# Kernel optimization log

Measured on AMD Instinct MI355X. Metric: run time of the kernel, lower is better.

The kernel has to match this reference:

```python
import jax, jax.numpy as jnp
import numpy as np

S = 1          # MD_S
R = 8          # MD_R
STEPS = 4      # MD_STEPS (train == eval)
INV_T = 1.0    # INV_T
EPS = 1e-6     # get_epsilon() for fp32, no params


def _build_estimators(D):
    # Smooth RBF basis bank: sigmas (6,8) stride 1, (12,15) stride 2, (18,24) stride 3, + ones column.
    t = jnp.arange(D, dtype=jnp.float32)[:, None]
    n = jnp.arange(D, dtype=jnp.float32)[None, :]
    dd = (t - n) ** 2
    cols = []
    for sig, stride in [(6.0, 1), (8.0, 1), (12.0, 2), (15.0, 2), (18.0, 3), (24.0, 3)]:
        rbf = jnp.exp(-0.5 * dd / (2.0 * sig * sig))
        cols.append(rbf[:, ::stride])
    cols.append(jnp.ones((D, 1), dtype=jnp.float32))
    return jnp.concatenate(cols, axis=1)  # [D, K], K = 589 for D = 160


def _l2_normalize(v, axis):
    # matches F.normalize(eps=1e-12)
    return v / jnp.maximum(jnp.linalg.norm(v, axis=axis, keepdims=True), 1e-12)


def _local_step(x, E, bases, coef):
    # NMF multiplicative update with smoothness estimators E (SNMF). x:[b,D,N], E:[b,D,K], bases:[b,K,R], coef:[b,N,R]
    Eb = jnp.einsum('bdk,bkr->bdr', E, bases)                      # [b,D,R]
    num_c = jnp.einsum('bdn,bdr->bnr', x, Eb)                      # x^T (E bases)
    den_c = jnp.einsum('bnr,brs->bns', coef, jnp.einsum('bdr,bds->brs', Eb, Eb))
    coef = coef * num_c / (den_c + EPS)
    num_b = jnp.einsum('bdk,bdr->bkr', E, jnp.einsum('bdn,bnr->bdr', x, coef))  # E^T (x coef)
    ctc = jnp.einsum('bnr,bns->brs', coef, coef)                   # [b,R,R]
    tmp = jnp.einsum('bdk,bkr->bdr', E, jnp.einsum('bkr,brs->bks', bases, ctc))
    den_b = jnp.einsum('bdk,bdr->bkr', E, tmp)                     # E^T E bases (coef^T coef)
    bases = bases * num_b / (den_b + EPS)
    return bases, coef


def _forward(x, bases_init):
    B, C, T, H, W = x.shape
    D = T // S
    N = C * H * W
    xr = x.reshape(B * S, D, N)                                    # same row-major view as torch .view
    E1 = _build_estimators(D)                                      # [D,K]
    E = jnp.broadcast_to(E1, (B * S,) + E1.shape)                  # [b,D,K]
    bases = _l2_normalize(bases_init, axis=1)                      # _build_bases: rand + normalize(dim=1)
    # local_inference (@torch.no_grad())
    Eb = jnp.einsum('bdk,bkr->bdr', E, bases)
    coef = jax.nn.softmax(INV_T * jnp.einsum('bdn,bdr->bnr', xr, Eb), axis=-1)
    for _ in range(STEPS):
        bases, coef = _local_step(xr, E, bases, coef)
    bases = jax.lax.stop_gradient(bases)
    coef = jax.lax.stop_gradient(coef)
    # compute_coef (differentiable single coef update)
    Eb = jnp.einsum('bdk,bkr->bdr', E, bases)
    num_c = jnp.einsum('bdn,bdr->bnr', xr, Eb)
    den_c = jnp.einsum('bnr,brs->bns', coef, jnp.einsum('bdr,bds->brs', Eb, Eb))
    coef = coef * num_c / (den_c + EPS)
    # reconstruction: (E bases) coef^T
    x_rec = jnp.einsum('bdr,bnr->bdn', Eb, coef)
    return x_rec.reshape(B, C, T, H, W)


def setup_inputs() -> dict:
    key = jax.random.key(0)
    k1, k2 = jax.random.split(key)
    B, C, T, H, W = 8, 32, 160, 32, 32
    D = T // S
    K = _build_estimators(D).shape[1]  # 589
    x = jax.random.uniform(k1, (B, C, T, H, W), dtype=jnp.float32)
    bases_init = jax.random.uniform(k2, (B * S, K, R), dtype=jnp.float32)
    return {"x": x, "bases_init": bases_init}


def reference(x, bases_init):
    return _forward(x, bases_init)
```

## Files before the change

### kernel.cpp

```cpp
#include <hip/hip_runtime.h>

#define DD   160
#define KKE  589
#define RR   8
#define NNX  32768
#define NB   8
#define EPSN 1e-6f

__global__ __launch_bounds__(256) void k_build(float* __restrict__ E, float* __restrict__ ET) {
    const int t = blockIdx.x;
    for (int j = threadIdx.x; j < KKE; j += 256) {
        float val;
        if (j == 588) {
            val = 1.f;
        } else {
            int n; float s2x4;
            if (j < 160)      { n = j;           s2x4 = 144.f;  }
            else if (j < 320) { n = j - 160;     s2x4 = 256.f;  }
            else if (j < 400) { n = 2*(j - 320); s2x4 = 576.f;  }
            else if (j < 480) { n = 2*(j - 400); s2x4 = 900.f;  }
            else if (j < 534) { n = 3*(j - 480); s2x4 = 1296.f; }
            else              { n = 3*(j - 534); s2x4 = 2304.f; }
            float d = (float)(t - n);
            val = expf(-(d * d) / s2x4);
        }
        E[t*KKE + j]  = val;
        ET[j*DD + t]  = val;
    }
}

template <bool NORM>
__global__ __launch_bounds__(256) void k_eb(const float* __restrict__ ET,
                                            const float* __restrict__ bsrc,
                                            float* __restrict__ bnorm_out,
                                            float* __restrict__ Eb_out,
                                            float* __restrict__ xc,
                                            float* __restrict__ ctc) {
    __shared__ float bcol[KKE];
    __shared__ float etch[64 * DD];
    __shared__ float red[4];
    const int tid = threadIdx.x;
    const int b = blockIdx.x >> 3;
    const int r = blockIdx.x & 7;

    const int k0 = tid, k1 = tid + 256, k2 = tid + 512;
    float v0 = bsrc[(b*KKE + k0)*RR + r];
    float v1 = bsrc[(b*KKE + k1)*RR + r];
    float v2 = (k2 < KKE) ? bsrc[(b*KKE + k2)*RR + r] : 0.f;

    if (NORM) {
        float ss = v0*v0 + v1*v1 + v2*v2;
        #pragma unroll
        for (int off = 32; off; off >>= 1) ss += __shfl_xor(ss, off);
        if ((tid & 63) == 0) red[tid >> 6] = ss;
        __syncthreads();
        float tot = red[0] + red[1] + red[2] + red[3];
        float scale = 1.f / fmaxf(sqrtf(tot), 1e-12f);
        v0 *= scale; v1 *= scale; v2 *= scale;
        bnorm_out[(b*KKE + k0)*RR + r] = v0;
        bnorm_out[(b*KKE + k1)*RR + r] = v1;
        if (k2 < KKE) bnorm_out[(b*KKE + k2)*RR + r] = v2;
    }
    bcol[k0] = v0; bcol[k1] = v1; if (k2 < KKE) bcol[k2] = v2;
    __syncthreads();

    float acc = 0.f;
    for (int c0 = 0; c0 < KKE; c0 += 64) {
        const int kcn = (KKE - c0 < 64) ? (KKE - c0) : 64;
        const int nf4 = kcn * (DD/4);
        for (int i4 = tid; i4 < nf4; i4 += 256)
            *(float4*)&etch[i4*4] = *(const float4*)&ET[c0*DD + i4*4];
        __syncthreads();
        if (tid < DD) {
            #pragma unroll 4
            for (int kk = 0; kk < kcn; ++kk)
                acc += etch[kk*DD + tid] * bcol[c0 + kk];
        }
        __syncthreads();
    }
    if (tid < DD) {
        Eb_out[b*DD*RR + tid*RR + r] = acc;
        xc[b*DD*RR + tid*RR + r] = 0.f;
    }
    if (tid < 8) ctc[b*64 + tid*8 + r] = 0.f;
}

template <bool FIRST>
__global__ __launch_bounds__(256) void k_step(const float* __restrict__ x,
                                              const float* __restrict__ Eb_g,
                                              float* __restrict__ coef,
                                              float* __restrict__ xc,
                                              float* __restrict__ ctc) {
    __shared__ float eb[DD*RR];
    __shared__ float ebteb[64];
    __shared__ float xt[64*161];
    __shared__ float pn[1536];

    const int tid = threadIdx.x;
    const int b = blockIdx.y;
    const int base_n = blockIdx.x * 256;

    for (int i = tid; i < DD*RR; i += 256) eb[i] = Eb_g[b*DD*RR + i];
    __syncthreads();
    if (tid < 64) {
        const int r = tid >> 3, s = tid & 7;
        float a = 0.f;
        #pragma unroll 4
        for (int d = 0; d < DD; ++d) a += eb[d*RR + r] * eb[d*RR + s];
        ebteb[tid] = a;
    }
    __syncthreads();

    float xcp[8] = {0,0,0,0,0,0,0,0};
    float ctcp = 0.f;

    const int q = tid >> 6;
    const int c = tid & 63;

    for (int st = 0; st < 4; ++st) {
        const int n0 = base_n + st*64;
        #pragma unroll
        for (int it = 0; it < 10; ++it) {
            const int idx = tid + it*256;
            const int row = idx >> 4;
            const int c4  = (idx & 15) << 2;
            const float4 v = *(const float4*)&x[(b*DD + row)*NNX + n0 + c4];
            xt[(c4+0)*161 + row] = v.x;
            xt[(c4+1)*161 + row] = v.y;
            xt[(c4+2)*161 + row] = v.z;
            xt[(c4+3)*161 + row] = v.w;
        }
        __syncthreads();
        float nc[8] = {0,0,0,0,0,0,0,0};
        {
            const int dbase = q*40;
            #pragma unroll 4
            for (int dd = 0; dd < 40; ++dd) {
                const int d = dbase + dd;
                const float xv = xt[c*161 + d];
                const float4 e0 = *(const float4*)&eb[d*RR];
                const float4 e1 = *(const float4*)&eb[d*RR + 4];
                nc[0] += xv*e0.x; nc[1] += xv*e0.y; nc[2] += xv*e0.z; nc[3] += xv*e0.w;
                nc[4] += xv*e1.x; nc[5] += xv*e1.y; nc[6] += xv*e1.z; nc[7] += xv*e1.w;
            }
        }
        if (q != 0) {
            #pragma unroll
            for (int r = 0; r < 8; ++r) pn[((q-1)*8 + r)*64 + c] = nc[r];
        }
        __syncthreads();
        if (tid < 64) {
            float num[8], cold[8];
            #pragma unroll
            for (int r = 0; r < 8; ++r)
                num[r] = nc[r] + pn[r*64 + tid] + pn[(8+r)*64 + tid] + pn[(16+r)*64 + tid];
            if (FIRST) {
                float m = num[0];
                #pragma unroll
                for (int r = 1; r < 8; ++r) m = fmaxf(m, num[r]);
                float ssum = 0.f;
                #pragma unroll
                for (int r = 0; r < 8; ++r) { cold[r] = expf(num[r] - m); ssum += cold[r]; }
                const float inv = 1.f / ssum;
                #pragma unroll
                for (int r = 0; r < 8; ++r) cold[r] *= inv;
            } else {
                const float4 u0 = *(const float4*)&coef[(b*NNX + n0 + tid)*RR];
                const float4 u1 = *(const float4*)&coef[(b*NNX + n0 + tid)*RR + 4];
                cold[0]=u0.x; cold[1]=u0.y; cold[2]=u0.z; cold[3]=u0.w;
                cold[4]=u1.x; cold[5]=u1.y; cold[6]=u1.z; cold[7]=u1.w;
            }
            float cn[8];
            #pragma unroll
            for (int r = 0; r < 8; ++r) {
                float den = 0.f;
                #pragma unroll
                for (int s = 0; s < 8; ++s) den += cold[s] * ebteb[s*8 + r];
                cn[r] = cold[r] * num[r] / (den + EPSN);
            }
            *(float4*)&coef[(b*NNX + n0 + tid)*RR]     = make_float4(cn[0],cn[1],cn[2],cn[3]);
            *(float4*)&coef[(b*NNX + n0 + tid)*RR + 4] = make_float4(cn[4],cn[5],cn[6],cn[7]);
            #pragma unroll
            for (int r = 0; r < 8; ++r) pn[tid*8 + r] = cn[r];
        }
        __syncthreads();
        if (tid >= 192) {
            const int r = (tid >> 3) & 7, s = tid & 7;
            #pragma unroll 4
            for (int i = 0; i < 64; ++i) {
                const int c2 = (i + tid) & 63;
                ctcp += pn[c2*8 + r] * pn[c2*8 + s];
            }
        }
        if (tid < DD) {
            #pragma unroll 4
            for (int n = 0; n < 64; ++n) {
                const float xv = xt[n*161 + tid];
                const float4 c0v = *(const float4*)&pn[n*8];
                const float4 c1v = *(const float4*)&pn[n*8 + 4];
                xcp[0] += xv*c0v.x; xcp[1] += xv*c0v.y; xcp[2] += xv*c0v.z; xcp[3] += xv*c0v.w;
                xcp[4] += xv*c1v.x; xcp[5] += xv*c1v.y; xcp[6] += xv*c1v.z; xcp[7] += xv*c1v.w;
            }
        }
        __syncthreads();
    }
    if (tid < DD) {
        #pragma unroll
        for (int r = 0; r < 8; ++r) atomicAdd(&xc[b*DD*RR + tid*RR + r], xcp[r]);
    }
    if (tid >= 192) {
        const int r = (tid >> 3) & 7, s = tid & 7;
        atomicAdd(&ctc[b*64 + r*8 + s], ctcp);
    }
}

__global__ __launch_bounds__(256) void k_bupd(const float* __restrict__ E,
                                              const float* __restrict__ Eb_old,
                                              const float* __restrict__ bases_old,
                                              const float* __restrict__ xc,
                                              const float* __restrict__ ctc,
                                              float* __restrict__ bases_new) {
    __shared__ float xcl[DD];
    __shared__ float tmp[DD];
    __shared__ float ctcc[8];
    const int tid = threadIdx.x;
    const int b = blockIdx.y >> 3;
    const int r = blockIdx.y & 7;
    if (tid < 8)  ctcc[tid] = ctc[b*64 + tid*8 + r];
    if (tid < DD) xcl[tid] = xc[b*DD*RR + tid*RR + r];
    __syncthreads();
    if (tid < DD) {
        float a = 0.f;
        #pragma unroll
        for (int s = 0; s < 8; ++s) a += Eb_old[b*DD*RR + tid*RR + s] * ctcc[s];
        tmp[tid] = a;
    }
    __syncthreads();
    const int k = blockIdx.x*256 + tid;
    if (k < KKE) {
        float nb = 0.f, db = 0.f;
        #pragma unroll 4
        for (int d = 0; d < DD; ++d) {
            const float e = E[d*KKE + k];
            nb += e * xcl[d];
            db += e * tmp[d];
        }
        const float bo = bases_old[(b*KKE + k)*RR + r];
        bases_new[(b*KKE + k)*RR + r] = bo * nb / (db + EPSN);
    }
}

__global__ __launch_bounds__(256) void k_final(const float* __restrict__ x,
                                               const float* __restrict__ Eb_g,
                                               const float* __restrict__ coef,
                                               float* __restrict__ out) {
    __shared__ float eb[DD*RR];
    __shared__ float ebteb[64];
    const int tid = threadIdx.x;
    const int b = blockIdx.y;
    const int n0 = blockIdx.x*512 + tid*2;

    for (int i = tid; i < DD*RR; i += 256) eb[i] = Eb_g[b*DD*RR + i];
    __syncthreads();
    if (tid < 64) {
        const int r = tid >> 3, s = tid & 7;
        float a = 0.f;
        #pragma unroll 4
        for (int d = 0; d < DD; ++d) a += eb[d*RR + r] * eb[d*RR + s];
        ebteb[tid] = a;
    }
    __syncthreads();

    float a0[8] = {0,0,0,0,0,0,0,0};
    float a1[8] = {0,0,0,0,0,0,0,0};
    #pragma unroll 4
    for (int d = 0; d < DD; ++d) {
        const float2 xv = *(const float2*)&x[(b*DD + d)*NNX + n0];
        const float4 e0 = *(const float4*)&eb[d*RR];
        const float4 e1 = *(const float4*)&eb[d*RR + 4];
        a0[0] += xv.x*e0.x; a0[1] += xv.x*e0.y; a0[2] += xv.x*e0.z; a0[3] += xv.x*e0.w;
        a0[4] += xv.x*e1.x; a0[5] += xv.x*e1.y; a0[6] += xv.x*e1.z; a0[7] += xv.x*e1.w;
        a1[0] += xv.y*e0.x; a1[1] += xv.y*e0.y; a1[2] += xv.y*e0.z; a1[3] += xv.y*e0.w;
        a1[4] += xv.y*e1.x; a1[5] += xv.y*e1.y; a1[6] += xv.y*e1.z; a1[7] += xv.y*e1.w;
    }
    const float* cp = &coef[(b*NNX + n0)*RR];
    const float4 u0 = ((const float4*)cp)[0];
    const float4 u1 = ((const float4*)cp)[1];
    const float4 u2 = ((const float4*)cp)[2];
    const float4 u3 = ((const float4*)cp)[3];
    const float c0a[8] = {u0.x,u0.y,u0.z,u0.w,u1.x,u1.y,u1.z,u1.w};
    const float c1a[8] = {u2.x,u2.y,u2.z,u2.w,u3.x,u3.y,u3.z,u3.w};
    float cf0[8], cf1[8];
    #pragma unroll
    for (int r = 0; r < 8; ++r) {
        float d0 = 0.f, d1 = 0.f;
        #pragma unroll
        for (int s = 0; s < 8; ++s) {
            const float t = ebteb[s*8 + r];
            d0 += c0a[s]*t; d1 += c1a[s]*t;
        }
        cf0[r] = c0a[r]*a0[r]/(d0 + EPSN);
        cf1[r] = c1a[r]*a1[r]/(d1 + EPSN);
    }
    #pragma unroll 4
    for (int d = 0; d < DD; ++d) {
        const float4 e0 = *(const float4*)&eb[d*RR];
        const float4 e1 = *(const float4*)&eb[d*RR + 4];
        float o0 = e0.x*cf0[0] + e0.y*cf0[1] + e0.z*cf0[2] + e0.w*cf0[3]
                 + e1.x*cf0[4] + e1.y*cf0[5] + e1.z*cf0[6] + e1.w*cf0[7];
        float o1 = e0.x*cf1[0] + e0.y*cf1[1] + e0.z*cf1[2] + e0.w*cf1[3]
                 + e1.x*cf1[4] + e1.y*cf1[5] + e1.z*cf1[6] + e1.w*cf1[7];
        *(float2*)&out[(b*DD + d)*NNX + n0] = make_float2(o0, o1);
    }
}

extern "C" void kernel_launch(void* const* d_in, const int* in_sizes, int n_in,
                              void* d_out, int out_size, void* d_ws, size_t ws_size,
                              hipStream_t stream) {
    const float* x     = (const float*)d_in[0];
    const float* binit = (const float*)d_in[1];
    float* out = (float*)d_out;

    float* w      = (float*)d_ws;
    float* E      = w;
    float* ET     = E      + DD*KKE;
    float* bases0 = ET     + DD*KKE;
    float* bases1 = bases0 + NB*KKE*RR;
    float* Eb0    = bases1 + NB*KKE*RR;
    float* Eb1    = Eb0    + NB*DD*RR;
    float* coef   = Eb1    + NB*DD*RR;
    float* xc     = coef   + (size_t)NB*NNX*RR;
    float* ctc    = xc     + NB*DD*RR;

    const dim3 gstep(128, 8), gbupd(3, 64), gfin(64, 8);

    k_build<<<160, 256, 0, stream>>>(E, ET);
    k_eb<true><<<64, 256, 0, stream>>>(ET, binit, bases0, Eb0, xc, ctc);

    k_step<true><<<gstep, 256, 0, stream>>>(x, Eb0, coef, xc, ctc);
    k_bupd<<<gbupd, 256, 0, stream>>>(E, Eb0, bases0, xc, ctc, bases1);
    k_eb<false><<<64, 256, 0, stream>>>(ET, bases1, bases1, Eb1, xc, ctc);
    k_step<false><<<gstep, 256, 0, stream>>>(x, Eb1, coef, xc, ctc);
    k_bupd<<<gbupd, 256, 0, stream>>>(E, Eb1, bases1, xc, ctc, bases0);
    k_eb<false><<<64, 256, 0, stream>>>(ET, bases0, bases0, Eb0, xc, ctc);
    k_step<false><<<gstep, 256, 0, stream>>>(x, Eb0, coef, xc, ctc);
    k_bupd<<<gbupd, 256, 0, stream>>>(E, Eb0, bases0, xc, ctc, bases1);
    k_eb<false><<<64, 256, 0, stream>>>(ET, bases1, bases1, Eb1, xc, ctc);
    k_step<false><<<gstep, 256, 0, stream>>>(x, Eb1, coef, xc, ctc);
    k_bupd<<<gbupd, 256, 0, stream>>>(E, Eb1, bases1, xc, ctc, bases0);
    k_eb<false><<<64, 256, 0, stream>>>(ET, bases0, bases0, Eb0, xc, ctc);
    k_final<<<gfin, 256, 0, stream>>>(x, Eb0, coef, out);
}
```

Measured before the change: 980.8 us.

## Split fused NMF step into separate coef and x·coef kernels with precomputed EbᵀEb

The fused per-step kernel, which staged a transposed x tile in shared memory and computed coef updates, ctc and x·coef together, is split into two streaming kernels. k_coef updates coef per column and reduces ctc with wave shuffles. k_xct recomputes x·coef by reading x a second time with register tiling. EbᵀEb is now computed once in the parallelised k_eb through atomics instead of in every block, and bases are updated in place. The aim is higher occupancy and fewer barriers, at the cost of reading x twice per iteration.

New measurement: 1.621 ms. 1.65x slower.

```diff
diff --git a/kernel.cpp b/kernel.cpp
--- a/kernel.cpp
+++ b/kernel.cpp
@@ -29,197 +29,217 @@
     }
 }
 
-template <bool NORM>
-__global__ __launch_bounds__(256) void k_eb(const float* __restrict__ ET,
-                                            const float* __restrict__ bsrc,
-                                            float* __restrict__ bnorm_out,
-                                            float* __restrict__ Eb_out,
-                                            float* __restrict__ xc,
-                                            float* __restrict__ ctc) {
-    __shared__ float bcol[KKE];
-    __shared__ float etch[64 * DD];
+__global__ __launch_bounds__(256) void k_norm(const float* __restrict__ bsrc,
+                                              float* __restrict__ bdst,
+                                              float* __restrict__ ebt) {
     __shared__ float red[4];
     const int tid = threadIdx.x;
     const int b = blockIdx.x >> 3;
     const int r = blockIdx.x & 7;
-
+    if (r == 0 && tid < 64) ebt[b*64 + tid] = 0.f;
     const int k0 = tid, k1 = tid + 256, k2 = tid + 512;
     float v0 = bsrc[(b*KKE + k0)*RR + r];
     float v1 = bsrc[(b*KKE + k1)*RR + r];
     float v2 = (k2 < KKE) ? bsrc[(b*KKE + k2)*RR + r] : 0.f;
-
-    if (NORM) {
-        float ss = v0*v0 + v1*v1 + v2*v2;
-        #pragma unroll
-        for (int off = 32; off; off >>= 1) ss += __shfl_xor(ss, off);
-        if ((tid & 63) == 0) red[tid >> 6] = ss;
-        __syncthreads();
-        float tot = red[0] + red[1] + red[2] + red[3];
-        float scale = 1.f / fmaxf(sqrtf(tot), 1e-12f);
-        v0 *= scale; v1 *= scale; v2 *= scale;
-        bnorm_out[(b*KKE + k0)*RR + r] = v0;
-        bnorm_out[(b*KKE + k1)*RR + r] = v1;
-        if (k2 < KKE) bnorm_out[(b*KKE + k2)*RR + r] = v2;
-    }
-    bcol[k0] = v0; bcol[k1] = v1; if (k2 < KKE) bcol[k2] = v2;
-    __syncthreads();
-
+    float ss = v0*v0 + v1*v1 + v2*v2;
+    #pragma unroll
+    for (int off = 32; off; off >>= 1) ss += __shfl_xor(ss, off);
+    if ((tid & 63) == 0) red[tid >> 6] = ss;
+    __syncthreads();
+    const float tot = red[0] + red[1] + red[2] + red[3];
+    const float scale = 1.f / fmaxf(sqrtf(tot), 1e-12f);
+    bdst[(b*KKE + k0)*RR + r] = v0*scale;
+    bdst[(b*KKE + k1)*RR + r] = v1*scale;
+    if (k2 < KKE) bdst[(b*KKE + k2)*RR + r] = v2*scale;
+}
+
+__global__ __launch_bounds__(256) void k_eb(const float* __restrict__ ET,
+                                            const float* __restrict__ bases,
+                                            float* __restrict__ Eb,
+                                            float* __restrict__ ebt,
+                                            float* __restrict__ xc,
+                                            float* __restrict__ ctc) {
+    __shared__ float bl[KKE*RR];
+    __shared__ float ebl[32*RR];
+    const int tid = threadIdx.x;
+    const int dc = blockIdx.x;
+    const int b  = blockIdx.y;
+
+    xc[b*DD*RR + dc*256 + tid] = 0.f;
+    if (dc == 0 && tid < 64) ctc[b*64 + tid] = 0.f;
+
+    const float4* bsrc4 = (const float4*)(bases + (size_t)b*KKE*RR);
+    for (int i = tid; i < (KKE*RR)/4; i += 256) ((float4*)bl)[i] = bsrc4[i];
+    __syncthreads();
+
+    const int dl = tid >> 3, r = tid & 7;
+    const int d = dc*32 + dl;
     float acc = 0.f;
-    for (int c0 = 0; c0 < KKE; c0 += 64) {
-        const int kcn = (KKE - c0 < 64) ? (KKE - c0) : 64;
-        const int nf4 = kcn * (DD/4);
-        for (int i4 = tid; i4 < nf4; i4 += 256)
-            *(float4*)&etch[i4*4] = *(const float4*)&ET[c0*DD + i4*4];
-        __syncthreads();
-        if (tid < DD) {
-            #pragma unroll 4
-            for (int kk = 0; kk < kcn; ++kk)
-                acc += etch[kk*DD + tid] * bcol[c0 + kk];
-        }
-        __syncthreads();
-    }
-    if (tid < DD) {
-        Eb_out[b*DD*RR + tid*RR + r] = acc;
-        xc[b*DD*RR + tid*RR + r] = 0.f;
-    }
-    if (tid < 8) ctc[b*64 + tid*8 + r] = 0.f;
+    #pragma unroll 4
+    for (int k = 0; k < KKE; ++k)
+        acc += ET[k*DD + d] * bl[k*8 + r];
+    Eb[b*DD*RR + d*RR + r] = acc;
+    ebl[dl*8 + r] = acc;
+    __syncthreads();
+    if (tid < 64) {
+        const int r2 = tid >> 3, s2 = tid & 7;
+        float p = 0.f;
+        #pragma unroll
+        for (int i = 0; i < 32; ++i) p += ebl[i*8 + r2] * ebl[i*8 + s2];
+        atomicAdd(&ebt[b*64 + r2*8 + s2], p);
+    }
 }
 
 template <bool FIRST>
-__global__ __launch_bounds__(256) void k_step(const float* __restrict__ x,
-                                              const float* __restrict__ Eb_g,
+__global__ __launch_bounds__(256) void k_coef(const float* __restrict__ x,
+                                              const float* __restrict__ Eb,
+                                              const float* __restrict__ ebt,
                                               float* __restrict__ coef,
-                                              float* __restrict__ xc,
                                               float* __restrict__ ctc) {
-    __shared__ float eb[DD*RR];
-    __shared__ float ebteb[64];
-    __shared__ float xt[64*161];
-    __shared__ float pn[1536];
-
     const int tid = threadIdx.x;
     const int b = blockIdx.y;
-    const int base_n = blockIdx.x * 256;
-
-    for (int i = tid; i < DD*RR; i += 256) eb[i] = Eb_g[b*DD*RR + i];
-    __syncthreads();
-    if (tid < 64) {
-        const int r = tid >> 3, s = tid & 7;
-        float a = 0.f;
-        #pragma unroll 4
-        for (int d = 0; d < DD; ++d) a += eb[d*RR + r] * eb[d*RR + s];
-        ebteb[tid] = a;
-    }
-    __syncthreads();
-
-    float xcp[8] = {0,0,0,0,0,0,0,0};
-    float ctcp = 0.f;
-
-    const int q = tid >> 6;
-    const int c = tid & 63;
-
-    for (int st = 0; st < 4; ++st) {
-        const int n0 = base_n + st*64;
-        #pragma unroll
-        for (int it = 0; it < 10; ++it) {
-            const int idx = tid + it*256;
-            const int row = idx >> 4;
-            const int c4  = (idx & 15) << 2;
-            const float4 v = *(const float4*)&x[(b*DD + row)*NNX + n0 + c4];
-            xt[(c4+0)*161 + row] = v.x;
-            xt[(c4+1)*161 + row] = v.y;
-            xt[(c4+2)*161 + row] = v.z;
-            xt[(c4+3)*161 + row] = v.w;
-        }
-        __syncthreads();
-        float nc[8] = {0,0,0,0,0,0,0,0};
-        {
-            const int dbase = q*40;
-            #pragma unroll 4
-            for (int dd = 0; dd < 40; ++dd) {
-                const int d = dbase + dd;
-                const float xv = xt[c*161 + d];
-                const float4 e0 = *(const float4*)&eb[d*RR];
-                const float4 e1 = *(const float4*)&eb[d*RR + 4];
-                nc[0] += xv*e0.x; nc[1] += xv*e0.y; nc[2] += xv*e0.z; nc[3] += xv*e0.w;
-                nc[4] += xv*e1.x; nc[5] += xv*e1.y; nc[6] += xv*e1.z; nc[7] += xv*e1.w;
+    const int n0 = blockIdx.x*512 + tid*2;
+    const float* __restrict__ ebg = Eb + b*DD*RR;
+    const float* __restrict__ xp  = x + (size_t)b*DD*NNX + n0;
+
+    float a0[8] = {0,0,0,0,0,0,0,0}, a1[8] = {0,0,0,0,0,0,0,0};
+    #pragma unroll 2
+    for (int d = 0; d < DD; ++d) {
+        const float2 xv = *(const float2*)(xp + (size_t)d*NNX);
+        float e[8];
+        *(float4*)&e[0] = *(const float4*)(ebg + d*RR);
+        *(float4*)&e[4] = *(const float4*)(ebg + d*RR + 4);
+        #pragma unroll
+        for (int r = 0; r < 8; ++r) { a0[r] += xv.x*e[r]; a1[r] += xv.y*e[r]; }
+    }
+
+    float c0[8], c1[8];
+    if (FIRST) {
+        float m0 = a0[0], m1 = a1[0];
+        #pragma unroll
+        for (int r = 1; r < 8; ++r) { m0 = fmaxf(m0, a0[r]); m1 = fmaxf(m1, a1[r]); }
+        float s0 = 0.f, s1 = 0.f;
+        #pragma unroll
+        for (int r = 0; r < 8; ++r) { c0[r] = expf(a0[r]-m0); s0 += c0[r];
+                                      c1[r] = expf(a1[r]-m1); s1 += c1[r]; }
+        const float i0 = 1.f/s0, i1 = 1.f/s1;
+        #pragma unroll
+        for (int r = 0; r < 8; ++r) { c0[r] *= i0; c1[r] *= i1; }
+    } else {
+        float* cp = coef + ((size_t)b*NNX + n0)*RR;
+        *(float4*)&c0[0] = *(const float4*)(cp);
+        *(float4*)&c0[4] = *(const float4*)(cp + 4);
+        *(float4*)&c1[0] = *(const float4*)(cp + 8);
+        *(float4*)&c1[4] = *(const float4*)(cp + 12);
+    }
+
+    const float* __restrict__ ebtp = ebt + b*64;
+    float d0[8] = {0,0,0,0,0,0,0,0}, d1[8] = {0,0,0,0,0,0,0,0};
+    #pragma unroll
+    for (int s = 0; s < 8; ++s) {
+        float e[8];
+        *(float4*)&e[0] = *(const float4*)(ebtp + s*8);
+        *(float4*)&e[4] = *(const float4*)(ebtp + s*8 + 4);
+        #pragma unroll
+        for (int r = 0; r < 8; ++r) { d0[r] += c0[s]*e[r]; d1[r] += c1[s]*e[r]; }
+    }
+    #pragma unroll
+    for (int r = 0; r < 8; ++r) {
+        c0[r] = c0[r]*a0[r]/(d0[r] + EPSN);
+        c1[r] = c1[r]*a1[r]/(d1[r] + EPSN);
+    }
+    {
+        float* cp = coef + ((size_t)b*NNX + n0)*RR;
+        *(float4*)(cp)      = *(float4*)&c0[0];
+        *(float4*)(cp + 4)  = *(float4*)&c0[4];
+        *(float4*)(cp + 8)  = *(float4*)&c1[0];
+        *(float4*)(cp + 12) = *(float4*)&c1[4];
+    }
+
+    float ctv[36];
+    #pragma unroll
+    for (int r = 0; r < 8; ++r) {
+        #pragma unroll
+        for (int s = r; s < 8; ++s)
+            ctv[r*8 + s - (r*(r+1))/2] = c0[r]*c0[s] + c1[r]*c1[s];
+    }
+    #pragma unroll
+    for (int off = 32; off; off >>= 1) {
+        #pragma unroll
+        for (int v = 0; v < 36; ++v) ctv[v] += __shfl_xor(ctv[v], off);
+    }
+    if ((tid & 63) == 0) {
+        #pragma unroll
+        for (int r = 0; r < 8; ++r) {
+            #pragma unroll
+            for (int s = r; s < 8; ++s) {
+                const float v = ctv[r*8 + s - (r*(r+1))/2];
+                atomicAdd(&ctc[b*64 + r*8 + s], v);
+                if (s != r) atomicAdd(&ctc[b*64 + s*8 + r], v);
             }
         }
-        if (q != 0) {
+    }
+}
+
+__global__ __launch_bounds__(320) void k_xct(const float* __restrict__ x,
+                                             const float* __restrict__ coef,
+                                             float* __restrict__ xc,
+                                             float* __restrict__ ebt) {
+    __shared__ float red[320*33];
+    const int tid = threadIdx.x;
+    const int b  = blockIdx.y;
+    const int n0 = blockIdx.x*512;
+    if (blockIdx.x == 0 && tid < 64) ebt[b*64 + tid] = 0.f;
+
+    const int dq = tid >> 3;
+    const int st = tid & 7;
+    const float* __restrict__ xb = x + (size_t)b*DD*NNX;
+    const float* __restrict__ cb = coef + (size_t)b*NNX*RR;
+
+    float acc[4][8] = {{0}};
+    for (int g = 0; g < 16; ++g) {
+        const int n = n0 + g*32 + st*4;
+        float c[4][8];
+        #pragma unroll
+        for (int j = 0; j < 4; ++j) {
+            *(float4*)&c[j][0] = *(const float4*)(cb + (size_t)(n+j)*RR);
+            *(float4*)&c[j][4] = *(const float4*)(cb + (size_t)(n+j)*RR + 4);
+        }
+        #pragma unroll
+        for (int i = 0; i < 4; ++i) {
+            float xv[4];
+            *(float4*)&xv[0] = *(const float4*)(xb + (size_t)(dq*4+i)*NNX + n);
             #pragma unroll
-            for (int r = 0; r < 8; ++r) pn[((q-1)*8 + r)*64 + c] = nc[r];
-        }
-        __syncthreads();
-        if (tid < 64) {
-            float num[8], cold[8];
-            #pragma unroll
-            for (int r = 0; r < 8; ++r)
-                num[r] = nc[r] + pn[r*64 + tid] + pn[(8+r)*64 + tid] + pn[(16+r)*64 + tid];
-            if (FIRST) {
-                float m = num[0];
+            for (int j = 0; j < 4; ++j) {
                 #pragma unroll
-                for (int r = 1; r < 8; ++r) m = fmaxf(m, num[r]);
-                float ssum = 0.f;
-                #pragma unroll
-                for (int r = 0; r < 8; ++r) { cold[r] = expf(num[r] - m); ssum += cold[r]; }
-                const float inv = 1.f / ssum;
-                #pragma unroll
-                for (int r = 0; r < 8; ++r) cold[r] *= inv;
-            } else {
-                const float4 u0 = *(const float4*)&coef[(b*NNX + n0 + tid)*RR];
-                const float4 u1 = *(const float4*)&coef[(b*NNX + n0 + tid)*RR + 4];
-                cold[0]=u0.x; cold[1]=u0.y; cold[2]=u0.z; cold[3]=u0.w;
-                cold[4]=u1.x; cold[5]=u1.y; cold[6]=u1.z; cold[7]=u1.w;
+                for (int r = 0; r < 8; ++r) acc[i][r] += xv[j]*c[j][r];
             }
-            float cn[8];
-            #pragma unroll
-            for (int r = 0; r < 8; ++r) {
-                float den = 0.f;
-                #pragma unroll
-                for (int s = 0; s < 8; ++s) den += cold[s] * ebteb[s*8 + r];
-                cn[r] = cold[r] * num[r] / (den + EPSN);
-            }
-            *(float4*)&coef[(b*NNX + n0 + tid)*RR]     = make_float4(cn[0],cn[1],cn[2],cn[3]);
-            *(float4*)&coef[(b*NNX + n0 + tid)*RR + 4] = make_float4(cn[4],cn[5],cn[6],cn[7]);
-            #pragma unroll
-            for (int r = 0; r < 8; ++r) pn[tid*8 + r] = cn[r];
-        }
-        __syncthreads();
-        if (tid >= 192) {
-            const int r = (tid >> 3) & 7, s = tid & 7;
-            #pragma unroll 4
-            for (int i = 0; i < 64; ++i) {
-                const int c2 = (i + tid) & 63;
-                ctcp += pn[c2*8 + r] * pn[c2*8 + s];
-            }
-        }
-        if (tid < DD) {
-            #pragma unroll 4
-            for (int n = 0; n < 64; ++n) {
-                const float xv = xt[n*161 + tid];
-                const float4 c0v = *(const float4*)&pn[n*8];
-                const float4 c1v = *(const float4*)&pn[n*8 + 4];
-                xcp[0] += xv*c0v.x; xcp[1] += xv*c0v.y; xcp[2] += xv*c0v.z; xcp[3] += xv*c0v.w;
-                xcp[4] += xv*c1v.x; xcp[5] += xv*c1v.y; xcp[6] += xv*c1v.z; xcp[7] += xv*c1v.w;
-            }
-        }
-        __syncthreads();
-    }
-    if (tid < DD) {
-        #pragma unroll
-        for (int r = 0; r < 8; ++r) atomicAdd(&xc[b*DD*RR + tid*RR + r], xcp[r]);
-    }
-    if (tid >= 192) {
-        const int r = (tid >> 3) & 7, s = tid & 7;
-        atomicAdd(&ctc[b*64 + r*8 + s], ctcp);
+        }
+    }
+    #pragma unroll
+    for (int v = 0; v < 32; ++v) red[tid*33 + v] = acc[v>>3][v&7];
+    __syncthreads();
+    {
+        const int dqr = tid >> 3, r = tid & 7;
+        float s0=0.f, s1=0.f, s2=0.f, s3=0.f;
+        #pragma unroll
+        for (int s = 0; s < 8; ++s) {
+            const float* rp = &red[(dqr*8 + s)*33];
+            s0 += rp[0*8 + r]; s1 += rp[1*8 + r]; s2 += rp[2*8 + r]; s3 += rp[3*8 + r];
+        }
+        float* xcp = &xc[b*DD*RR + (dqr*4)*RR + r];
+        atomicAdd(xcp + 0,  s0);
+        atomicAdd(xcp + 8,  s1);
+        atomicAdd(xcp + 16, s2);
+        atomicAdd(xcp + 24, s3);
     }
 }
 
 __global__ __launch_bounds__(256) void k_bupd(const float* __restrict__ E,
-                                              const float* __restrict__ Eb_old,
-                                              const float* __restrict__ bases_old,
+                                              const float* __restrict__ Eb,
+                                              float* __restrict__ bases,
                                               const float* __restrict__ xc,
-                                              const float* __restrict__ ctc,
-                                              float* __restrict__ bases_new) {
+                                              const float* __restrict__ ctc) {
     __shared__ float xcl[DD];
     __shared__ float tmp[DD];
     __shared__ float ctcc[8];
@@ -232,7 +252,7 @@
     if (tid < DD) {
         float a = 0.f;
         #pragma unroll
-        for (int s = 0; s < 8; ++s) a += Eb_old[b*DD*RR + tid*RR + s] * ctcc[s];
+        for (int s = 0; s < 8; ++s) a += Eb[b*DD*RR + tid*RR + s] * ctcc[s];
         tmp[tid] = a;
     }
     __syncthreads();
@@ -245,72 +265,65 @@
             nb += e * xcl[d];
             db += e * tmp[d];
         }
-        const float bo = bases_old[(b*KKE + k)*RR + r];
-        bases_new[(b*KKE + k)*RR + r] = bo * nb / (db + EPSN);
+        const float bo = bases[(b*KKE + k)*RR + r];
+        bases[(b*KKE + k)*RR + r] = bo * nb / (db + EPSN);
     }
 }
 
 __global__ __launch_bounds__(256) void k_final(const float* __restrict__ x,
-                                               const float* __restrict__ Eb_g,
+                                               const float* __restrict__ Eb,
+                                               const float* __restrict__ ebt,
                                                const float* __restrict__ coef,
                                                float* __restrict__ out) {
-    __shared__ float eb[DD*RR];
-    __shared__ float ebteb[64];
     const int tid = threadIdx.x;
     const int b = blockIdx.y;
     const int n0 = blockIdx.x*512 + tid*2;
-
-    for (int i = tid; i < DD*RR; i += 256) eb[i] = Eb_g[b*DD*RR + i];
-    __syncthreads();
-    if (tid < 64) {
-        const int r = tid >> 3, s = tid & 7;
-        float a = 0.f;
-        #pragma unroll 4
-        for (int d = 0; d < DD; ++d) a += eb[d*RR + r] * eb[d*RR + s];
-        ebteb[tid] = a;
-    }
-    __syncthreads();
-
-    float a0[8] = {0,0,0,0,0,0,0,0};
-    float a1[8] = {0,0,0,0,0,0,0,0};
-    #pragma unroll 4
+    const float* __restrict__ ebg = Eb + b*DD*RR;
+    const float* __restrict__ xp  = x + (size_t)b*DD*NNX + n0;
+
+    float a0[8] = {0,0,0,0,0,0,0,0}, a1[8] = {0,0,0,0,0,0,0,0};
+    #pragma unroll 2
     for (int d = 0; d < DD; ++d) {
-        const float2 xv = *(const float2*)&x[(b*DD + d)*NNX + n0];
-        const float4 e0 = *(const float4*)&eb[d*RR];
-        const float4 e1 = *(const float4*)&eb[d*RR + 4];
-        a0[0] += xv.x*e0.x; a0[1] += xv.x*e0.y; a0[2] += xv.x*e0.z; a0[3] += xv.x*e0.w;
-        a0[4] += xv.x*e1.x; a0[5] += xv.x*e1.y; a0[6] += xv.x*e1.z; a0[7] += xv.x*e1.w;
-        a1[0] += xv.y*e0.x; a1[1] += xv.y*e0.y; a1[2] += xv.y*e0.z; a1[3] += xv.y*e0.w;
-        a1[4] += xv.y*e1.x; a1[5] += xv.y*e1.y; a1[6] += xv.y*e1.z; a1[7] += xv.y*e1.w;
-    }
-    const float* cp = &coef[(b*NNX + n0)*RR];
-    const float4 u0 = ((const float4*)cp)[0];
-    const float4 u1 = ((const float4*)cp)[1];
-    const float4 u2 = ((const float4*)cp)[2];
-    const float4 u3 = ((const float4*)cp)[3];
-    const float c0a[8] = {u0.x,u0.y,u0.z,u0.w,u1.x,u1.y,u1.z,u1.w};
-    const float c1a[8] = {u2.x,u2.y,u2.z,u2.w,u3.x,u3.y,u3.z,u3.w};
-    float cf0[8], cf1[8];
+        const float2 xv = *(const float2*)(xp + (size_t)d*NNX);
+        float e[8];
+        *(float4*)&e[0] = *(const float4*)(ebg + d*RR);
+        *(float4*)&e[4] = *(const float4*)(ebg + d*RR + 4);
+        #pragma unroll
+        for (int r = 0; r < 8; ++r) { a0[r] += xv.x*e[r]; a1[r] += xv.y*e[r]; }
+    }
+    float c0[8], c1[8];
+    {
+        const float* cp = coef + ((size_t)b*NNX + n0)*RR;
+        *(float4*)&c0[0] = *(const float4*)(cp);
+        *(float4*)&c0[4] = *(const float4*)(cp + 4);
+        *(float4*)&c1[0] = *(const float4*)(cp + 8);
+        *(float4*)&c1[4] = *(const float4*)(cp + 12);
+    }
+    const float* __restrict__ ebtp = ebt + b*64;
+    float d0[8] = {0,0,0,0,0,0,0,0}, d1[8] = {0,0,0,0,0,0,0,0};
+    #pragma unroll
+    for (int s = 0; s < 8; ++s) {
+        float e[8];
+        *(float4*)&e[0] = *(const float4*)(ebtp + s*8);
+        *(float4*)&e[4] = *(const float4*)(ebtp + s*8 + 4);
+        #pragma unroll
+        for (int r = 0; r < 8; ++r) { d0[r] += c0[s]*e[r]; d1[r] += c1[s]*e[r]; }
+    }
     #pragma unroll
     for (int r = 0; r < 8; ++r) {
-        float d0 = 0.f, d1 = 0.f;
-        #pragma unroll
-        for (int s = 0; s < 8; ++s) {
-            const float t = ebteb[s*8 + r];
-            d0 += c0a[s]*t; d1 += c1a[s]*t;
-        }
-        cf0[r] = c0a[r]*a0[r]/(d0 + EPSN);
-        cf1[r] = c1a[r]*a1[r]/(d1 + EPSN);
-    }
-    #pragma unroll 4
+        c0[r] = c0[r]*a0[r]/(d0[r] + EPSN);
+        c1[r] = c1[r]*a1[r]/(d1[r] + EPSN);
+    }
+    float* op = (float*)out + (size_t)b*DD*NNX + n0;
+    #pragma unroll 2
     for (int d = 0; d < DD; ++d) {
-        const float4 e0 = *(const float4*)&eb[d*RR];
-        const float4 e1 = *(const float4*)&eb[d*RR + 4];
-        float o0 = e0.x*cf0[0] + e0.y*cf0[1] + e0.z*cf0[2] + e0.w*cf0[3]
-                 + e1.x*cf0[4] + e1.y*cf0[5] + e1.z*cf0[6] + e1.w*cf0[7];
-        float o1 = e0.x*cf1[0] + e0.y*cf1[1] + e0.z*cf1[2] + e0.w*cf1[3]
-                 + e1.x*cf1[4] + e1.y*cf1[5] + e1.z*cf1[6] + e1.w*cf1[7];
-        *(float2*)&out[(b*DD + d)*NNX + n0] = make_float2(o0, o1);
+        float e[8];
+        *(float4*)&e[0] = *(const float4*)(ebg + d*RR);
+        *(float4*)&e[4] = *(const float4*)(ebg + d*RR + 4);
+        float o0 = 0.f, o1 = 0.f;
+        #pragma unroll
+        for (int r = 0; r < 8; ++r) { o0 += e[r]*c0[r]; o1 += e[r]*c1[r]; }
+        *(float2*)(op + (size_t)d*NNX) = make_float2(o0, o1);
     }
 }
 
@@ -324,30 +337,34 @@
     float* w      = (float*)d_ws;
     float* E      = w;
     float* ET     = E      + DD*KKE;
-    float* bases0 = ET     + DD*KKE;
-    float* bases1 = bases0 + NB*KKE*RR;
-    float* Eb0    = bases1 + NB*KKE*RR;
-    float* Eb1    = Eb0    + NB*DD*RR;
-    float* coef   = Eb1    + NB*DD*RR;
+    float* bases  = ET     + DD*KKE;
+    float* Eb     = bases  + NB*KKE*RR;
+    float* ebt    = Eb     + NB*DD*RR;
+    float* coef   = ebt    + NB*64;
     float* xc     = coef   + (size_t)NB*NNX*RR;
     float* ctc    = xc     + NB*DD*RR;
 
-    const dim3 gstep(128, 8), gbupd(3, 64), gfin(64, 8);
+    const dim3 g_eb(5, 8), g_cf(64, 8), g_xc(64, 8), g_bu(3, 64), g_fin(64, 8);
 
     k_build<<<160, 256, 0, stream>>>(E, ET);
-    k_eb<true><<<64, 256, 0, stream>>>(ET, binit, bases0, Eb0, xc, ctc);
-
-    k_step<true><<<gstep, 256, 0, stream>>>(x, Eb0, coef, xc, ctc);
-    k_bupd<<<gbupd, 256, 0, stream>>>(E, Eb0, bases0, xc, ctc, bases1);
-    k_eb<false><<<64, 256, 0, stream>>>(ET, bases1, bases1, Eb1, xc, ctc);
-    k_step<false><<<gstep, 256, 0, stream>>>(x, Eb1, coef, xc, ctc);
-    k_bupd<<<gbupd, 256, 0, stream>>>(E, Eb1, bases1, xc, ctc, bases0);
-    k_eb<false><<<64, 256, 0, stream>>>(ET, bases0, bases0, Eb0, xc, ctc);
-    k_step<false><<<gstep, 256, 0, stream>>>(x, Eb0, coef, xc, ctc);
-    k_bupd<<<gbupd, 256, 0, stream>>>(E, Eb0, bases0, xc, ctc, bases1);
-    k_eb<false><<<64, 256, 0, stream>>>(ET, bases1, bases1, Eb1, xc, ctc);
-    k_step<false><<<gstep, 256, 0, stream>>>(x, Eb1, coef, xc, ctc);
-    k_bupd<<<gbupd, 256, 0, stream>>>(E, Eb1, bases1, xc, ctc, bases0);
-    k_eb<false><<<64, 256, 0, stream>>>(ET, bases0, bases0, Eb0, xc, ctc);
-    k_final<<<gfin, 256, 0, stream>>>(x, Eb0, coef, out);
-}
+    k_norm<<<64, 256, 0, stream>>>(binit, bases, ebt);
+    k_eb<<<g_eb, 256, 0, stream>>>(ET, bases, Eb, ebt, xc, ctc);
+
+    k_coef<true><<<g_cf, 256, 0, stream>>>(x, Eb, ebt, coef, ctc);
+    k_xct<<<g_xc, 320, 0, stream>>>(x, coef, xc, ebt);
+    k_bupd<<<g_bu, 256, 0, stream>>>(E, Eb, bases, xc, ctc);
+    k_eb<<<g_eb, 256, 0, stream>>>(ET, bases, Eb, ebt, xc, ctc);
+    k_coef<false><<<g_cf, 256, 0, stream>>>(x, Eb, ebt, coef, ctc);
+    k_xct<<<g_xc, 320, 0, stream>>>(x, coef, xc, ebt);
+    k_bupd<<<g_bu, 256, 0, stream>>>(E, Eb, bases, xc, ctc);
+    k_eb<<<g_eb, 256, 0, stream>>>(ET, bases, Eb, ebt, xc, ctc);
+    k_coef<false><<<g_cf, 256, 0, stream>>>(x, Eb, ebt, coef, ctc);
+    k_xct<<<g_xc, 320, 0, stream>>>(x, coef, xc, ebt);
+    k_bupd<<<g_bu, 256, 0, stream>>>(E, Eb, bases, xc, ctc);
+    k_eb<<<g_eb, 256, 0, stream>>>(ET, bases, Eb, ebt, xc, ctc);
+    k_coef<false><<<g_cf, 256, 0, stream>>>(x, Eb, ebt, coef, ctc);
+    k_xct<<<g_xc, 320, 0, stream>>>(x, coef, xc, ebt);
+    k_bupd<<<g_bu, 256, 0, stream>>>(E, Eb, bases, xc, ctc);
+    k_eb<<<g_eb, 256, 0, stream>>>(ET, bases, Eb, ebt, xc, ctc);
+    k_final<<<g_fin, 256, 0, stream>>>(x, Eb, ebt, coef, out);
+}
```
